# Kernel optimization log

Measured on AMD Instinct MI355X. Metric: run time of the kernel, lower is better.

Reference implementation:

```python
import jax, jax.numpy as jnp
import numpy as np

N_HIDDEN = 8
N_CLASSES = 10
TIME_STEPS = 28
INPUT_DIM = 28
FORGET_BIAS = 1.0


def setup_inputs() -> dict:
    key = jax.random.key(0)
    k1, k2, k3, k4 = jax.random.split(key, 4)
    B = 32768
    x = jax.random.normal(k1, (B, TIME_STEPS, INPUT_DIM), dtype=jnp.float32)
    # BasicLSTMCell kernel: [input_dim + hidden, 4*hidden], gate order i, j, f, o
    W_lstm = jax.random.normal(k2, (INPUT_DIM + N_HIDDEN, 4 * N_HIDDEN), dtype=jnp.float32) * 0.1
    b_lstm = jnp.zeros((4 * N_HIDDEN,), dtype=jnp.float32)  # TF zero-init bias
    out_weights = jax.random.normal(k3, (N_HIDDEN, N_CLASSES), dtype=jnp.float32)
    out_biases = jax.random.normal(k4, (N_CLASSES,), dtype=jnp.float32)
    return {"x": x, "W_lstm": W_lstm, "b_lstm": b_lstm,
            "out_weights": out_weights, "out_biases": out_biases}


def reference(x, W_lstm, b_lstm, out_weights, out_biases):
    B = x.shape[0]

    def step(carry, xt):
        c, h = carry
        gates = jnp.concatenate([xt, h], axis=-1) @ W_lstm + b_lstm  # [B, 4H]
        i, j, f, o = jnp.split(gates, 4, axis=-1)  # BasicLSTMCell order: i, j, f, o
        new_c = c * jax.nn.sigmoid(f + FORGET_BIAS) + jax.nn.sigmoid(i) * jnp.tanh(j)
        new_h = jnp.tanh(new_c) * jax.nn.sigmoid(o)
        return (new_c, new_h), None

    xs = jnp.swapaxes(x, 0, 1)  # [T, B, input_dim]
    init = (jnp.zeros((B, N_HIDDEN), x.dtype), jnp.zeros((B, N_HIDDEN), x.dtype))
    (_, last_h), _ = jax.lax.scan(step, init, xs)
    logits = last_h @ out_weights + out_biases  # [B, n_classes]
    return logits
```

## Files before the change

kernel.cpp:

```cpp
#include <hip/hip_runtime.h>


#define TSTEPS 28
#define DIN    28
#define NH     8
#define NG     32
#define NC     10
#define EPB    8
#define XQ_PER_ELEM (TSTEPS * 7)

__device__ __forceinline__ float fexp2(float x) { return __builtin_amdgcn_exp2f(x); }
__device__ __forceinline__ float frcp(float x)  { return __builtin_amdgcn_rcpf(x); }

#define SWZ(v, imm) \
    __int_as_float(__builtin_amdgcn_ds_swizzle(__float_as_int(v), (imm)))

__device__ __forceinline__ float dpp_ror1(float v) {
    int i = __float_as_int(v);
    return __int_as_float(
        __builtin_amdgcn_update_dpp(i, i, 0x121, 0xF, 0xF, true));
}

__global__ __launch_bounds__(256, 6) void lstm_kernel(
    const float* __restrict__ x,
    const float* __restrict__ W,
    const float* __restrict__ bias,
    const float* __restrict__ Wout,
    const float* __restrict__ bout,
    float* __restrict__ out)
{
    __shared__ float4 xs[EPB * XQ_PER_ELEM];

    const int g   = threadIdx.x >> 5;
    const int l5  = threadIdx.x & 31;
    const int u   = l5 & 7;
    const int gt  = l5 >> 3;
    const int e   = blockIdx.x * EPB + g;

    {
        const float4* gx = (const float4*)(x + (size_t)blockIdx.x *
                                           (EPB * TSTEPS * DIN));
#pragma unroll
        for (int i = 0; i < 7; ++i) {
            int idx = threadIdx.x + i * 256;
            if (idx < EPB * XQ_PER_ELEM) xs[idx] = gx[idx];
        }
    }

    float Wx[DIN];
#pragma unroll
    for (int k = 0; k < DIN; ++k) Wx[k] = W[k * NG + l5];
    float Wh[NH];
#pragma unroll
    for (int s = 0; s < NH; ++s)
        Wh[s] = W[(DIN + ((u - s + 8) & 7)) * NG + l5];
#pragma unroll
    for (int k = 0; k < DIN; ++k) asm volatile("" : "+v"(Wx[k]));
#pragma unroll
    for (int s = 0; s < NH; ++s) asm volatile("" : "+v"(Wh[s]));

    const float bg = bias[l5] + (gt == 2 ? 1.0f : 0.0f);
    const float sK = (gt == 1) ?  2.8853900817779268f : -1.4426950408889634f;
    const float mK = (gt == 1) ? -2.0f : 1.0f;
    const float qK = (gt == 1) ?  1.0f : 0.0f;

    float c = 0.0f;
    float hprev = 0.0f;

    __syncthreads();

    const float4* xrow = xs + g * XQ_PER_ELEM;

#pragma unroll 2
    for (int t = 0; t < TSTEPS; ++t) {
        float4 xq[7];
#pragma unroll
        for (int i = 0; i < 7; ++i) xq[i] = xrow[t * 7 + i];

        float g0 = bg, g1 = 0.0f, g2 = 0.0f, g3 = 0.0f;
#pragma unroll
        for (int i = 0; i < 7; ++i) {
            g0 = fmaf(xq[i].x, Wx[4*i+0], g0);
            g1 = fmaf(xq[i].y, Wx[4*i+1], g1);
            g2 = fmaf(xq[i].z, Wx[4*i+2], g2);
            g3 = fmaf(xq[i].w, Wx[4*i+3], g3);
        }

        {
            float hc = hprev;
            g0 = fmaf(hc, Wh[0], g0);
            hc = dpp_ror1(hc); g1 = fmaf(hc, Wh[1], g1);
            hc = dpp_ror1(hc); g2 = fmaf(hc, Wh[2], g2);
            hc = dpp_ror1(hc); g3 = fmaf(hc, Wh[3], g3);
            hc = dpp_ror1(hc); g0 = fmaf(hc, Wh[4], g0);
            hc = dpp_ror1(hc); g1 = fmaf(hc, Wh[5], g1);
            hc = dpp_ror1(hc); g2 = fmaf(hc, Wh[6], g2);
            hc = dpp_ror1(hc); g3 = fmaf(hc, Wh[7], g3);
        }
        float gsum = (g0 + g1) + (g2 + g3);

        float a = fmaf(mK, frcp(1.0f + fexp2(sK * gsum)), qK);

        float iv = SWZ(a, 0x0007);
        float jv = SWZ(a, 0x0107);
        float fv = SWZ(a, 0x0207);
        float ov = SWZ(a, 0x0307);

        c = fmaf(c, fv, iv * jv);
        float th = fmaf(-2.0f,
                        frcp(1.0f + fexp2(2.8853900817779268f * c)),
                        1.0f);
        hprev = th * ov;
    }

    float hall[NH];
    hall[0] = SWZ(hprev, 0x0000);
    hall[1] = SWZ(hprev, 0x0020);
    hall[2] = SWZ(hprev, 0x0040);
    hall[3] = SWZ(hprev, 0x0060);
    hall[4] = SWZ(hprev, 0x0080);
    hall[5] = SWZ(hprev, 0x00A0);
    hall[6] = SWZ(hprev, 0x00C0);
    hall[7] = SWZ(hprev, 0x00E0);

    if (l5 < NC) {
        float acc = bout[l5];
#pragma unroll
        for (int k = 0; k < NH; ++k)
            acc = fmaf(hall[k], Wout[k * NC + l5], acc);
        out[(size_t)e * NC + l5] = acc;
    }
}

extern "C" void kernel_launch(void* const* d_in, const int* in_sizes, int n_in,
                              void* d_out, int out_size, void* d_ws, size_t ws_size,
                              hipStream_t stream) {
    const float* x    = (const float*)d_in[0];
    const float* W    = (const float*)d_in[1];
    const float* b    = (const float*)d_in[2];
    const float* Wout = (const float*)d_in[3];
    const float* bout = (const float*)d_in[4];
    float* out = (float*)d_out;

    const int B = in_sizes[0] / (TSTEPS * DIN);
    const int grid = B / EPB;
    lstm_kernel<<<grid, 256, 0, stream>>>(x, W, b, Wout, bout, out);
}
```

Measured before the change: 182.7 us.

## Map each batch element to 16 lanes computing two gate columns per lane

Each thread now computes two gate columns (m and m+16), so one batch element uses 16 lanes instead of 32 and a 256-thread block handles 16 elements. The cross-gate exchange moves from four LDS swizzles to two DPP row-xor-8 moves plus selects. The shared x buffer gets a padded stride of 197 float4 per element, presumably to reduce LDS bank conflicts. The trade is about double the per-lane weight registers, which lowers the occupancy hint from 6 to 4, and an index division in the staging loop.

```diff
diff --git a/kernel.cpp b/kernel.cpp
--- a/kernel.cpp
+++ b/kernel.cpp
@@ -6,8 +6,8 @@
 #define NH     8
 #define NG     32
 #define NC     10
-#define EPB    8
-#define XQ_PER_ELEM (TSTEPS * 7)
+#define EPB    16
+#define XF4    197
 
 __device__ __forceinline__ float fexp2(float x) { return __builtin_amdgcn_exp2f(x); }
 __device__ __forceinline__ float frcp(float x)  { return __builtin_amdgcn_rcpf(x); }
@@ -20,8 +20,13 @@
     return __int_as_float(
         __builtin_amdgcn_update_dpp(i, i, 0x121, 0xF, 0xF, true));
 }
+__device__ __forceinline__ float dpp_xor8(float v) {
+    int i = __float_as_int(v);
+    return __int_as_float(
+        __builtin_amdgcn_update_dpp(i, i, 0x128, 0xF, 0xF, true));
+}
 
-__global__ __launch_bounds__(256, 6) void lstm_kernel(
+__global__ __launch_bounds__(256, 4) void lstm_kernel(
     const float* __restrict__ x,
     const float* __restrict__ W,
     const float* __restrict__ bias,
@@ -29,47 +34,60 @@
     const float* __restrict__ bout,
     float* __restrict__ out)
 {
-    __shared__ float4 xs[EPB * XQ_PER_ELEM];
+    __shared__ float4 xs[EPB * XF4];
 
-    const int g   = threadIdx.x >> 5;
-    const int l5  = threadIdx.x & 31;
-    const int u   = l5 & 7;
-    const int gt  = l5 >> 3;
-    const int e   = blockIdx.x * EPB + g;
+    const int  eb   = threadIdx.x >> 4;
+    const int  m    = threadIdx.x & 15;
+    const int  u    = m & 7;
+    const bool lowm = (m < 8);
+    const int  e    = blockIdx.x * EPB + eb;
 
     {
         const float4* gx = (const float4*)(x + (size_t)blockIdx.x *
                                            (EPB * TSTEPS * DIN));
-#pragma unroll
-        for (int i = 0; i < 7; ++i) {
-            int idx = threadIdx.x + i * 256;
-            if (idx < EPB * XQ_PER_ELEM) xs[idx] = gx[idx];
+        for (int idx = threadIdx.x; idx < EPB * 196; idx += 256) {
+            int el = idx / 196, r = idx - el * 196;
+            xs[el * XF4 + r] = gx[idx];
         }
     }
 
-    float Wx[DIN];
+    const int col_lo = m, col_hi = m + 16;
+    float Wx0[DIN], Wx1[DIN];
 #pragma unroll
-    for (int k = 0; k < DIN; ++k) Wx[k] = W[k * NG + l5];
-    float Wh[NH];
+    for (int k = 0; k < DIN; ++k) {
+        Wx0[k] = W[k * NG + col_lo];
+        Wx1[k] = W[k * NG + col_hi];
+    }
+    float Wh0[NH], Wh1[NH];
 #pragma unroll
-    for (int s = 0; s < NH; ++s)
-        Wh[s] = W[(DIN + ((u - s + 8) & 7)) * NG + l5];
+    for (int s = 0; s < NH; ++s) {
+        int r = DIN + ((u - s + 8) & 7);
+        Wh0[s] = W[r * NG + col_lo];
+        Wh1[s] = W[r * NG + col_hi];
+    }
 #pragma unroll
-    for (int k = 0; k < DIN; ++k) asm volatile("" : "+v"(Wx[k]));
+    for (int k = 0; k < DIN; ++k) {
+        asm volatile("" : "+v"(Wx0[k]));
+        asm volatile("" : "+v"(Wx1[k]));
+    }
 #pragma unroll
-    for (int s = 0; s < NH; ++s) asm volatile("" : "+v"(Wh[s]));
+    for (int s = 0; s < NH; ++s) {
+        asm volatile("" : "+v"(Wh0[s]));
+        asm volatile("" : "+v"(Wh1[s]));
+    }
 
-    const float bg = bias[l5] + (gt == 2 ? 1.0f : 0.0f);
-    const float sK = (gt == 1) ?  2.8853900817779268f : -1.4426950408889634f;
-    const float mK = (gt == 1) ? -2.0f : 1.0f;
-    const float qK = (gt == 1) ?  1.0f : 0.0f;
+    const float bg_lo = bias[col_lo];
+    const float bg_hi = bias[col_hi] + (lowm ? 1.0f : 0.0f);
+    const float sK = lowm ? -1.4426950408889634f :  2.8853900817779268f;
+    const float mK = lowm ?  1.0f                : -2.0f;
+    const float qK = lowm ?  0.0f                :  1.0f;
 
     float c = 0.0f;
     float hprev = 0.0f;
 
     __syncthreads();
 
-    const float4* xrow = xs + g * XQ_PER_ELEM;
+    const float4* xrow = xs + eb * XF4;
 
 #pragma unroll 2
     for (int t = 0; t < TSTEPS; ++t) {
@@ -77,36 +95,51 @@
 #pragma unroll
         for (int i = 0; i < 7; ++i) xq[i] = xrow[t * 7 + i];
 
-        float g0 = bg, g1 = 0.0f, g2 = 0.0f, g3 = 0.0f;
+        float g0 = bg_lo, g1 = 0.0f, g2 = 0.0f, g3 = 0.0f;
+        float G0 = bg_hi, G1 = 0.0f, G2 = 0.0f, G3 = 0.0f;
 #pragma unroll
         for (int i = 0; i < 7; ++i) {
-            g0 = fmaf(xq[i].x, Wx[4*i+0], g0);
-            g1 = fmaf(xq[i].y, Wx[4*i+1], g1);
-            g2 = fmaf(xq[i].z, Wx[4*i+2], g2);
-            g3 = fmaf(xq[i].w, Wx[4*i+3], g3);
+            g0 = fmaf(xq[i].x, Wx0[4*i+0], g0);
+            G0 = fmaf(xq[i].x, Wx1[4*i+0], G0);
+            g1 = fmaf(xq[i].y, Wx0[4*i+1], g1);
+            G1 = fmaf(xq[i].y, Wx1[4*i+1], G1);
+            g2 = fmaf(xq[i].z, Wx0[4*i+2], g2);
+            G2 = fmaf(xq[i].z, Wx1[4*i+2], G2);
+            g3 = fmaf(xq[i].w, Wx0[4*i+3], g3);
+            G3 = fmaf(xq[i].w, Wx1[4*i+3], G3);
         }
 
         {
             float hc = hprev;
-            g0 = fmaf(hc, Wh[0], g0);
-            hc = dpp_ror1(hc); g1 = fmaf(hc, Wh[1], g1);
-            hc = dpp_ror1(hc); g2 = fmaf(hc, Wh[2], g2);
-            hc = dpp_ror1(hc); g3 = fmaf(hc, Wh[3], g3);
-            hc = dpp_ror1(hc); g0 = fmaf(hc, Wh[4], g0);
-            hc = dpp_ror1(hc); g1 = fmaf(hc, Wh[5], g1);
-            hc = dpp_ror1(hc); g2 = fmaf(hc, Wh[6], g2);
-            hc = dpp_ror1(hc); g3 = fmaf(hc, Wh[7], g3);
+            g0 = fmaf(hc, Wh0[0], g0); G0 = fmaf(hc, Wh1[0], G0);
+            hc = dpp_ror1(hc);
+            g1 = fmaf(hc, Wh0[1], g1); G1 = fmaf(hc, Wh1[1], G1);
+            hc = dpp_ror1(hc);
+            g2 = fmaf(hc, Wh0[2], g2); G2 = fmaf(hc, Wh1[2], G2);
+            hc = dpp_ror1(hc);
+            g3 = fmaf(hc, Wh0[3], g3); G3 = fmaf(hc, Wh1[3], G3);
+            hc = dpp_ror1(hc);
+            g0 = fmaf(hc, Wh0[4], g0); G0 = fmaf(hc, Wh1[4], G0);
+            hc = dpp_ror1(hc);
+            g1 = fmaf(hc, Wh0[5], g1); G1 = fmaf(hc, Wh1[5], G1);
+            hc = dpp_ror1(hc);
+            g2 = fmaf(hc, Wh0[6], g2); G2 = fmaf(hc, Wh1[6], G2);
+            hc = dpp_ror1(hc);
+            g3 = fmaf(hc, Wh0[7], g3); G3 = fmaf(hc, Wh1[7], G3);
         }
-        float gsum = (g0 + g1) + (g2 + g3);
+        float glo = (g0 + g1) + (g2 + g3);
+        float ghi = (G0 + G1) + (G2 + G3);
 
-        float a = fmaf(mK, frcp(1.0f + fexp2(sK * gsum)), qK);
+        float a_lo = fmaf(mK, frcp(1.0f + fexp2(sK * glo)), qK);
+        float a_hi = frcp(1.0f + fexp2(-1.4426950408889634f * ghi));
 
-        float iv = SWZ(a, 0x0007);
-        float jv = SWZ(a, 0x0107);
-        float fv = SWZ(a, 0x0207);
-        float ov = SWZ(a, 0x0307);
+        float p_lo = dpp_xor8(a_lo);
+        float p_hi = dpp_xor8(a_hi);
 
-        c = fmaf(c, fv, iv * jv);
+        float fv = lowm ? a_hi : p_hi;
+        float ov = lowm ? p_hi : a_hi;
+
+        c = fmaf(c, fv, a_lo * p_lo);
         float th = fmaf(-2.0f,
                         frcp(1.0f + fexp2(2.8853900817779268f * c)),
                         1.0f);
@@ -114,21 +147,21 @@
     }
 
     float hall[NH];
-    hall[0] = SWZ(hprev, 0x0000);
-    hall[1] = SWZ(hprev, 0x0020);
-    hall[2] = SWZ(hprev, 0x0040);
-    hall[3] = SWZ(hprev, 0x0060);
-    hall[4] = SWZ(hprev, 0x0080);
-    hall[5] = SWZ(hprev, 0x00A0);
-    hall[6] = SWZ(hprev, 0x00C0);
-    hall[7] = SWZ(hprev, 0x00E0);
+    hall[0] = SWZ(hprev, 0x0010);
+    hall[1] = SWZ(hprev, 0x0030);
+    hall[2] = SWZ(hprev, 0x0050);
+    hall[3] = SWZ(hprev, 0x0070);
+    hall[4] = SWZ(hprev, 0x0090);
+    hall[5] = SWZ(hprev, 0x00B0);
+    hall[6] = SWZ(hprev, 0x00D0);
+    hall[7] = SWZ(hprev, 0x00F0);
 
-    if (l5 < NC) {
-        float acc = bout[l5];
+    if (m < NC) {
+        float acc = bout[m];
 #pragma unroll
         for (int k = 0; k < NH; ++k)
-            acc = fmaf(hall[k], Wout[k * NC + l5], acc);
-        out[(size_t)e * NC + l5] = acc;
+            acc = fmaf(hall[k], Wout[k * NC + m], acc);
+        out[(size_t)e * NC + m] = acc;
     }
 }
 
```

After: 182.5 us. No clear change (-0.1%).
